# Kernel tuning notes

Measured on AMD Instinct MI355X. Metric: run time of the kernel, lower is better.

The kernel has to match this reference:

```python
import jax, jax.numpy as jnp
import numpy as np

Q, N, D, L = 4096, 50000, 5, 2


def setup_inputs() -> dict:
    key = jax.random.key(0)
    k1, k2, k3 = jax.random.split(key, 3)
    rss = jax.random.normal(k1, (Q, D), dtype=jnp.float32)
    Radio = jax.random.normal(k2, (N, D), dtype=jnp.float32)
    Loc = jax.random.normal(k3, (N, L), dtype=jnp.float32)
    sigma = jnp.ones((1,), dtype=jnp.float32)
    return {"rss": rss, "Radio": Radio, "Loc": Loc, "sigma": sigma}


def reference(rss, Radio, Loc, sigma):
    # x: [Q, 5] queries; Radio: [N, 5] reference fingerprints; Loc: [N, 2]
    x = rss.reshape(-1, D)
    # squared pairwise distances via the expanded form (no [Q,N,D] intermediate)
    x2 = jnp.sum(x * x, axis=-1, keepdims=True)            # [Q, 1]
    r2 = jnp.sum(Radio * Radio, axis=-1)                   # [N]
    d2 = x2 - 2.0 * (x @ Radio.T) + r2                     # [Q, N]
    d2 = jnp.maximum(d2, 0.0)
    sim = jnp.exp(-d2 / (2.0 * sigma[0] * sigma[0]))       # RBF kernel [Q, N]
    w = sim / jnp.sum(sim, axis=-1, keepdims=True)         # row-normalize
    l_hat = jnp.einsum('qn,nl->ql', w, Loc)                # Nadaraya-Watson [Q, 2]
    return l_hat
```

## Files before the change

### kernel.cpp

```cpp
#include <hip/hip_runtime.h>
#include <hip/hip_bf16.h>
#include <math.h>

#define QTOT   4096
#define NTOT   50000
#define NTILES 3125
#define NS     64
#define NB     16
#define QG     64
#define MAINBLOCKS (QG * NB)

#define BOFF   0u
#define BSIZE  (3125u * 512u)
#define AOFF   (BOFF + BSIZE)
#define ASIZE  (4096u * 32u)
#define ZOFF   (AOFF + ASIZE)
#define PARTOFF (ZOFF + 256u)

typedef unsigned short ushort_t;
typedef short  s16x8 __attribute__((ext_vector_type(8)));
typedef float  f32x4 __attribute__((ext_vector_type(4)));
typedef float  f2    __attribute__((ext_vector_type(2)));

#if __has_builtin(__builtin_amdgcn_exp2f)
#define EXP2F(x) __builtin_amdgcn_exp2f(x)
#else
#define EXP2F(x) exp2f(x)
#endif

static __device__ __forceinline__ f2 fma2(f2 a, f2 b, f2 c) {
#if __has_builtin(__builtin_elementwise_fma)
    return __builtin_elementwise_fma(a, b, c);
#else
    f2 r; r.x = fmaf(a.x, b.x, c.x); r.y = fmaf(a.y, b.y, c.y); return r;
#endif
}

static __device__ __forceinline__ void bsplit(float f, ushort_t& h, ushort_t& l) {
    __hip_bfloat16 hb = __float2bfloat16(f);
    float hf = __bfloat162float(hb);
    __hip_bfloat16 lb = __float2bfloat16(f - hf);
    h = *reinterpret_cast<ushort_t*>(&hb);
    l = *reinterpret_cast<ushort_t*>(&lb);
}

__global__ __launch_bounds__(256) void sknn_prep(
    const float* __restrict__ rss, const float* __restrict__ Radio,
    const float* __restrict__ sigma, char* __restrict__ ws)
{
    const int p = blockIdx.x * 256 + threadIdx.x;
    const float sg = sigma[0];
    const float g  = 1.4426950408889634f / (2.0f * sg * sg);
    const float g2 = 2.0f * g;

    if (p < NTOT) {
        float b[8]; float rr = 0.f;
        #pragma unroll
        for (int d = 0; d < 5; ++d) { float r = Radio[p*5+d]; b[d] = g2*r; rr += r*r; }
        b[5] = 1.0f; b[6] = -g * rr; b[7] = 0.0f;
        union { ushort_t u[8]; f32x4 v; } hi, lo;
        #pragma unroll
        for (int k = 0; k < 8; ++k) bsplit(b[k], hi.u[k], lo.u[k]);
        const int nt = p >> 4, nsub = p & 15;
        *(f32x4*)(ws + BOFF + (unsigned)nt*512u + (unsigned)nsub*16u)        = hi.v;
        *(f32x4*)(ws + BOFF + (unsigned)nt*512u + 256u + (unsigned)nsub*16u) = lo.v;
    }
    if (p < QTOT) {
        float a[8]; float xx = 0.f;
        #pragma unroll
        for (int d = 0; d < 5; ++d) { float x = rss[p*5+d]; a[d] = x; xx += x*x; }
        a[5] = -g * xx; a[6] = 1.0f; a[7] = 0.0f;
        union { ushort_t u[8]; f32x4 v; } hi, lo;
        #pragma unroll
        for (int k = 0; k < 8; ++k) bsplit(a[k], hi.u[k], lo.u[k]);
        *(f32x4*)(ws + AOFF + (unsigned)p*32u)       = hi.v;
        *(f32x4*)(ws + AOFF + (unsigned)p*32u + 16u) = lo.v;
    }
    if (p < 16) *(f32x4*)(ws + ZOFF + (unsigned)p*16u) = (f32x4){0.f,0.f,0.f,0.f};
}

__global__ __launch_bounds__(256, 4) void sknn_main(
    const char* __restrict__ tbl, const float* __restrict__ Loc,
    float* __restrict__ part)
{
    const int tid  = threadIdx.x;
    const int lane = tid & 63;
    const int w    = tid >> 6;
    const int qg   = blockIdx.x & (QG - 1);
    const int nb   = blockIdx.x >> 6;
    const int ns   = nb * 4 + w;
    const int qbase = qg * 64;
    const int j  = lane & 15;
    const int qd = lane >> 4;

    const unsigned abase = (qd == 3) ? (ZOFF + (unsigned)j*16u)
        : (AOFF + (unsigned)(qbase + j)*32u + (qd == 2 ? 16u : 0u));
    const unsigned astep = (qd == 3) ? 0u : 512u;
    const s16x8 a0 = *(const s16x8*)(tbl + abase);
    const s16x8 a1 = *(const s16x8*)(tbl + abase + astep);
    const s16x8 a2 = *(const s16x8*)(tbl + abase + 2u*astep);
    const s16x8 a3 = *(const s16x8*)(tbl + abase + 3u*astep);

    unsigned bofs = (qd == 3) ? (ZOFF + (unsigned)j*16u)
        : (BOFF + (unsigned)ns*512u + (qd == 1 ? 256u : 0u) + (unsigned)j*16u);
    const unsigned bstep = (qd == 3) ? 0u : (512u * NS);

    unsigned lofs = (unsigned)(ns*16 + j) * 8u;
    const char* locb = (const char*)Loc;

    f2 sm2[8]; f2 o[16];
    #pragma unroll
    for (int k = 0; k < 8;  ++k) sm2[k] = (f2){0.f, 0.f};
    #pragma unroll
    for (int k = 0; k < 16; ++k) o[k]   = (f2){0.f, 0.f};
    const f32x4 zz = {0.f, 0.f, 0.f, 0.f};

    s16x8 bcur = *(const s16x8*)(tbl + bofs);
    f2    lcur = *(const f2*)(locb + lofs);

    for (int nt = ns; nt < NTILES; nt += NS) {
        const bool has = (nt + NS) < NTILES;
        const unsigned bn = bofs + (has ? bstep : 0u);
        const unsigned ln = lofs + (has ? (unsigned)(NS*16*8) : 0u);
        const s16x8 bnx = *(const s16x8*)(tbl + bn);
        const f2    lnx = *(const f2*)(locb + ln);

        f32x4 t[4];
        t[0] = __builtin_amdgcn_mfma_f32_16x16x32_bf16(a0, bcur, zz, 0, 0, 0);
        t[1] = __builtin_amdgcn_mfma_f32_16x16x32_bf16(a1, bcur, zz, 0, 0, 0);
        t[2] = __builtin_amdgcn_mfma_f32_16x16x32_bf16(a2, bcur, zz, 0, 0, 0);
        t[3] = __builtin_amdgcn_mfma_f32_16x16x32_bf16(a3, bcur, zz, 0, 0, 0);

        #pragma unroll
        for (int qt = 0; qt < 4; ++qt) {
            const float s0 = EXP2F(t[qt][0]);
            const float s1 = EXP2F(t[qt][1]);
            const float s2 = EXP2F(t[qt][2]);
            const float s3 = EXP2F(t[qt][3]);
            sm2[qt*2+0] += (f2){s0, s1};
            sm2[qt*2+1] += (f2){s2, s3};
            o[qt*4+0] = fma2((f2){s0, s0}, lcur, o[qt*4+0]);
            o[qt*4+1] = fma2((f2){s1, s1}, lcur, o[qt*4+1]);
            o[qt*4+2] = fma2((f2){s2, s2}, lcur, o[qt*4+2]);
            o[qt*4+3] = fma2((f2){s3, s3}, lcur, o[qt*4+3]);
        }
        bcur = bnx; lcur = lnx; bofs = bn; lofs = ln;
    }

    #pragma unroll
    for (int m = 1; m <= 8; m <<= 1) {
        #pragma unroll
        for (int k = 0; k < 8; ++k) {
            sm2[k].x += __shfl_xor(sm2[k].x, m, 64);
            sm2[k].y += __shfl_xor(sm2[k].y, m, 64);
        }
        #pragma unroll
        for (int k = 0; k < 16; ++k) {
            o[k].x += __shfl_xor(o[k].x, m, 64);
            o[k].y += __shfl_xor(o[k].y, m, 64);
        }
    }

    __shared__ float red[4][3][64];
    #pragma unroll
    for (int qt = 0; qt < 4; ++qt) {
        #pragma unroll
        for (int i = 0; i < 4; ++i) {
            if (j == qt*4 + i) {
                const int ql = qt*16 + qd*4 + i;
                red[w][0][ql] = (i & 1) ? sm2[qt*2 + (i>>1)].y
                                        : sm2[qt*2 + (i>>1)].x;
                red[w][1][ql] = o[qt*4+i].x;
                red[w][2][ql] = o[qt*4+i].y;
            }
        }
    }
    __syncthreads();

    if (tid < 192) {
        const int comp = tid >> 6, ql = tid & 63;
        const float v = red[0][comp][ql] + red[1][comp][ql]
                      + red[2][comp][ql] + red[3][comp][ql];
        part[((nb * 3 + comp) << 12) + qbase + ql] = v;
    }
}

__global__ __launch_bounds__(256) void sknn_fin(
    const float* __restrict__ part, float* __restrict__ out)
{
    const int q = blockIdx.x * 256 + threadIdx.x;
    float s = 0.f, w0 = 0.f, w1 = 0.f;
    #pragma unroll
    for (int nb = 0; nb < NB; ++nb) {
        s  += part[((nb * 3 + 0) << 12) + q];
        w0 += part[((nb * 3 + 1) << 12) + q];
        w1 += part[((nb * 3 + 2) << 12) + q];
    }
    const float inv = 1.0f / s;
    out[q * 2 + 0] = w0 * inv;
    out[q * 2 + 1] = w1 * inv;
}

extern "C" void kernel_launch(void* const* d_in, const int* in_sizes, int n_in,
                              void* d_out, int out_size, void* d_ws, size_t ws_size,
                              hipStream_t stream) {
    const float* rss   = (const float*)d_in[0];
    const float* Radio = (const float*)d_in[1];
    const float* Loc   = (const float*)d_in[2];
    const float* sigma = (const float*)d_in[3];
    float* out  = (float*)d_out;
    char*  ws   = (char*)d_ws;
    float* part = (float*)(ws + PARTOFF);

    sknn_prep<<<(NTOT + 255) / 256, dim3(256), 0, stream>>>(rss, Radio, sigma, ws);
    sknn_main<<<MAINBLOCKS, dim3(256), 0, stream>>>(ws, Loc, part);
    sknn_fin<<<QTOT / 256, dim3(256), 0, stream>>>(part, out);
}
```

Before: 104.9 us.

## Move weighted Loc accumulation and row sums onto a second bf16 MFMA

```diff
diff --git a/kernel.cpp b/kernel.cpp
--- a/kernel.cpp
+++ b/kernel.cpp
@@ -9,18 +9,23 @@
 #define NB     16
 #define QG     64
 #define MAINBLOCKS (QG * NB)
+#define ASTEP_IT  (512u * NS)
+#define LTSTEP_IT (160u * NS)
+#define PREPN  (NTILES * 20)
 
 #define BOFF   0u
 #define BSIZE  (3125u * 512u)
 #define AOFF   (BOFF + BSIZE)
 #define ASIZE  (4096u * 32u)
 #define ZOFF   (AOFF + ASIZE)
-#define PARTOFF (ZOFF + 256u)
+#define LTOFF  (ZOFF + 256u)
+#define LTSIZE (3125u * 160u)
+#define PARTOFF (LTOFF + LTSIZE)
 
 typedef unsigned short ushort_t;
 typedef short  s16x8 __attribute__((ext_vector_type(8)));
+typedef short  s16x4 __attribute__((ext_vector_type(4)));
 typedef float  f32x4 __attribute__((ext_vector_type(4)));
-typedef float  f2    __attribute__((ext_vector_type(2)));
 
 #if __has_builtin(__builtin_amdgcn_exp2f)
 #define EXP2F(x) __builtin_amdgcn_exp2f(x)
@@ -28,13 +33,11 @@
 #define EXP2F(x) exp2f(x)
 #endif
 
-static __device__ __forceinline__ f2 fma2(f2 a, f2 b, f2 c) {
-#if __has_builtin(__builtin_elementwise_fma)
-    return __builtin_elementwise_fma(a, b, c);
+#if __has_builtin(__builtin_amdgcn_mfma_f32_16x16x16_bf16)
+#define MFMA16(a,b,c) __builtin_amdgcn_mfma_f32_16x16x16_bf16(a,b,c,0,0,0)
 #else
-    f2 r; r.x = fmaf(a.x, b.x, c.x); r.y = fmaf(a.y, b.y, c.y); return r;
+#define MFMA16(a,b,c) __builtin_amdgcn_mfma_f32_16x16x16bf16_1k(a,b,c,0,0,0)
 #endif
-}
 
 static __device__ __forceinline__ void bsplit(float f, ushort_t& h, ushort_t& l) {
     __hip_bfloat16 hb = __float2bfloat16(f);
@@ -44,9 +47,15 @@
     l = *reinterpret_cast<ushort_t*>(&lb);
 }
 
+static __device__ __forceinline__ ushort_t b16(float f) {
+    __hip_bfloat16 hb = __float2bfloat16(f);
+    return *reinterpret_cast<ushort_t*>(&hb);
+}
+
 __global__ __launch_bounds__(256) void sknn_prep(
     const float* __restrict__ rss, const float* __restrict__ Radio,
-    const float* __restrict__ sigma, char* __restrict__ ws)
+    const float* __restrict__ Loc, const float* __restrict__ sigma,
+    char* __restrict__ ws)
 {
     const int p = blockIdx.x * 256 + threadIdx.x;
     const float sg = sigma[0];
@@ -76,103 +85,117 @@
         *(f32x4*)(ws + AOFF + (unsigned)p*32u)       = hi.v;
         *(f32x4*)(ws + AOFF + (unsigned)p*32u + 16u) = lo.v;
     }
+    if (p < PREPN) {
+        const int T = p / 20;
+        const int c = p - T * 20;
+        const int m = c >> 2, qq = c & 3;
+        union { ushort_t u[4]; s16x4 v; } e;
+        #pragma unroll
+        for (int i = 0; i < 4; ++i) {
+            const int n = T*16 + qq*4 + i;
+            ushort_t h, l, val;
+            if (m == 0)      { bsplit(Loc[n*2+0], h, l); val = h; }
+            else if (m == 1) { bsplit(Loc[n*2+0], h, l); val = l; }
+            else if (m == 2) { bsplit(Loc[n*2+1], h, l); val = h; }
+            else if (m == 3) { bsplit(Loc[n*2+1], h, l); val = l; }
+            else             { val = b16(1.0f); }
+            e.u[i] = val;
+        }
+        *(s16x4*)(ws + LTOFF + (unsigned)T*160u + (unsigned)c*8u) = e.v;
+    }
     if (p < 16) *(f32x4*)(ws + ZOFF + (unsigned)p*16u) = (f32x4){0.f,0.f,0.f,0.f};
 }
 
+static __device__ __forceinline__ f32x4 step2(
+    const f32x4 t, const s16x4 lt, f32x4 c)
+{
+    const float s0 = EXP2F(t[0]);
+    const float s1 = EXP2F(t[1]);
+    const float s2 = EXP2F(t[2]);
+    const float s3 = EXP2F(t[3]);
+    union { ushort_t u[4]; s16x4 v; } bs;
+    bs.u[0] = b16(s0); bs.u[1] = b16(s1); bs.u[2] = b16(s2); bs.u[3] = b16(s3);
+    return MFMA16(lt, bs.v, c);
+}
+
 __global__ __launch_bounds__(256, 4) void sknn_main(
-    const char* __restrict__ tbl, const float* __restrict__ Loc,
-    float* __restrict__ part)
+    const char* __restrict__ tbl, float* __restrict__ part)
 {
     const int tid  = threadIdx.x;
     const int lane = tid & 63;
     const int w    = tid >> 6;
-    const int qg   = blockIdx.x & (QG - 1);
-    const int nb   = blockIdx.x >> 6;
+    const int nb   = blockIdx.x & (NB - 1);
+    const int qg   = blockIdx.x >> 4;
     const int ns   = nb * 4 + w;
     const int qbase = qg * 64;
     const int j  = lane & 15;
     const int qd = lane >> 4;
 
-    const unsigned abase = (qd == 3) ? (ZOFF + (unsigned)j*16u)
-        : (AOFF + (unsigned)(qbase + j)*32u + (qd == 2 ? 16u : 0u));
-    const unsigned astep = (qd == 3) ? 0u : 512u;
-    const s16x8 a0 = *(const s16x8*)(tbl + abase);
-    const s16x8 a1 = *(const s16x8*)(tbl + abase + astep);
-    const s16x8 a2 = *(const s16x8*)(tbl + abase + 2u*astep);
-    const s16x8 a3 = *(const s16x8*)(tbl + abase + 3u*astep);
-
-    unsigned bofs = (qd == 3) ? (ZOFF + (unsigned)j*16u)
-        : (BOFF + (unsigned)ns*512u + (qd == 1 ? 256u : 0u) + (unsigned)j*16u);
-    const unsigned bstep = (qd == 3) ? 0u : (512u * NS);
-
-    unsigned lofs = (unsigned)(ns*16 + j) * 8u;
-    const char* locb = (const char*)Loc;
-
-    f2 sm2[8]; f2 o[16];
+    const unsigned qb = (qd == 3) ? (ZOFF + (unsigned)j*16u)
+        : (AOFF + (unsigned)(qbase + j)*32u + (qd == 1 ? 16u : 0u));
+    const unsigned qs = (qd == 3) ? 0u : 512u;
+    const s16x8 bq0 = *(const s16x8*)(tbl + qb);
+    const s16x8 bq1 = *(const s16x8*)(tbl + qb + qs);
+    const s16x8 bq2 = *(const s16x8*)(tbl + qb + 2u*qs);
+    const s16x8 bq3 = *(const s16x8*)(tbl + qb + 3u*qs);
+
+    unsigned aofs = (qd == 3) ? (ZOFF + (unsigned)j*16u)
+        : (BOFF + (unsigned)ns*512u + (qd == 2 ? 256u : 0u) + (unsigned)j*16u);
+    const unsigned astep = (qd == 3) ? 0u : ASTEP_IT;
+
+    unsigned ltofs = (j < 5) ? (LTOFF + (unsigned)ns*160u + (unsigned)(j*4+qd)*8u)
+                             : ZOFF;
+    const unsigned ltstep = (j < 5) ? LTSTEP_IT : 0u;
+
+    f32x4 c2[4];
     #pragma unroll
-    for (int k = 0; k < 8;  ++k) sm2[k] = (f2){0.f, 0.f};
-    #pragma unroll
-    for (int k = 0; k < 16; ++k) o[k]   = (f2){0.f, 0.f};
+    for (int k = 0; k < 4; ++k) c2[k] = (f32x4){0.f, 0.f, 0.f, 0.f};
     const f32x4 zz = {0.f, 0.f, 0.f, 0.f};
 
-    s16x8 bcur = *(const s16x8*)(tbl + bofs);
-    f2    lcur = *(const f2*)(locb + lofs);
-
-    for (int nt = ns; nt < NTILES; nt += NS) {
-        const bool has = (nt + NS) < NTILES;
-        const unsigned bn = bofs + (has ? bstep : 0u);
-        const unsigned ln = lofs + (has ? (unsigned)(NS*16*8) : 0u);
-        const s16x8 bnx = *(const s16x8*)(tbl + bn);
-        const f2    lnx = *(const f2*)(locb + ln);
-
-        f32x4 t[4];
-        t[0] = __builtin_amdgcn_mfma_f32_16x16x32_bf16(a0, bcur, zz, 0, 0, 0);
-        t[1] = __builtin_amdgcn_mfma_f32_16x16x32_bf16(a1, bcur, zz, 0, 0, 0);
-        t[2] = __builtin_amdgcn_mfma_f32_16x16x32_bf16(a2, bcur, zz, 0, 0, 0);
-        t[3] = __builtin_amdgcn_mfma_f32_16x16x32_bf16(a3, bcur, zz, 0, 0, 0);
-
+    s16x8 acur = *(const s16x8*)(tbl + aofs);
+    s16x4 lcur = *(const s16x4*)(tbl + ltofs);
+
+    int nt = ns;
+    while (nt + NS < NTILES) {
+        aofs  += astep;
+        ltofs += ltstep;
+        const s16x8 anx = *(const s16x8*)(tbl + aofs);
+        const s16x4 lnx = *(const s16x4*)(tbl + ltofs);
+
+        const f32x4 t0 = __builtin_amdgcn_mfma_f32_16x16x32_bf16(acur, bq0, zz, 0, 0, 0);
+        const f32x4 t1 = __builtin_amdgcn_mfma_f32_16x16x32_bf16(acur, bq1, zz, 0, 0, 0);
+        const f32x4 t2 = __builtin_amdgcn_mfma_f32_16x16x32_bf16(acur, bq2, zz, 0, 0, 0);
+        const f32x4 t3 = __builtin_amdgcn_mfma_f32_16x16x32_bf16(acur, bq3, zz, 0, 0, 0);
+        c2[0] = step2(t0, lcur, c2[0]);
+        c2[1] = step2(t1, lcur, c2[1]);
+        c2[2] = step2(t2, lcur, c2[2]);
+        c2[3] = step2(t3, lcur, c2[3]);
+
+        acur = anx; lcur = lnx;
+        nt += NS;
+    }
+    {
+        const f32x4 t0 = __builtin_amdgcn_mfma_f32_16x16x32_bf16(acur, bq0, zz, 0, 0, 0);
+        const f32x4 t1 = __builtin_amdgcn_mfma_f32_16x16x32_bf16(acur, bq1, zz, 0, 0, 0);
+        const f32x4 t2 = __builtin_amdgcn_mfma_f32_16x16x32_bf16(acur, bq2, zz, 0, 0, 0);
+        const f32x4 t3 = __builtin_amdgcn_mfma_f32_16x16x32_bf16(acur, bq3, zz, 0, 0, 0);
+        c2[0] = step2(t0, lcur, c2[0]);
+        c2[1] = step2(t1, lcur, c2[1]);
+        c2[2] = step2(t2, lcur, c2[2]);
+        c2[3] = step2(t3, lcur, c2[3]);
+    }
+
+    __shared__ float red[4][3][64];
+    if (qd == 0) {
         #pragma unroll
         for (int qt = 0; qt < 4; ++qt) {
-            const float s0 = EXP2F(t[qt][0]);
-            const float s1 = EXP2F(t[qt][1]);
-            const float s2 = EXP2F(t[qt][2]);
-            const float s3 = EXP2F(t[qt][3]);
-            sm2[qt*2+0] += (f2){s0, s1};
-            sm2[qt*2+1] += (f2){s2, s3};
-            o[qt*4+0] = fma2((f2){s0, s0}, lcur, o[qt*4+0]);
-            o[qt*4+1] = fma2((f2){s1, s1}, lcur, o[qt*4+1]);
-            o[qt*4+2] = fma2((f2){s2, s2}, lcur, o[qt*4+2]);
-            o[qt*4+3] = fma2((f2){s3, s3}, lcur, o[qt*4+3]);
+            red[w][1][qt*16 + j] = c2[qt][0] + c2[qt][1];
+            red[w][2][qt*16 + j] = c2[qt][2] + c2[qt][3];
         }
-        bcur = bnx; lcur = lnx; bofs = bn; lofs = ln;
-    }
-
-    #pragma unroll
-    for (int m = 1; m <= 8; m <<= 1) {
-        #pragma unroll
-        for (int k = 0; k < 8; ++k) {
-            sm2[k].x += __shfl_xor(sm2[k].x, m, 64);
-            sm2[k].y += __shfl_xor(sm2[k].y, m, 64);
-        }
-        #pragma unroll
-        for (int k = 0; k < 16; ++k) {
-            o[k].x += __shfl_xor(o[k].x, m, 64);
-            o[k].y += __shfl_xor(o[k].y, m, 64);
-        }
-    }
-
-    __shared__ float red[4][3][64];
-    #pragma unroll
-    for (int qt = 0; qt < 4; ++qt) {
-        #pragma unroll
-        for (int i = 0; i < 4; ++i) {
-            if (j == qt*4 + i) {
-                const int ql = qt*16 + qd*4 + i;
-                red[w][0][ql] = (i & 1) ? sm2[qt*2 + (i>>1)].y
-                                        : sm2[qt*2 + (i>>1)].x;
-                red[w][1][ql] = o[qt*4+i].x;
-                red[w][2][ql] = o[qt*4+i].y;
-            }
+    } else if (qd == 1) {
+        #pragma unroll
+        for (int qt = 0; qt < 4; ++qt) {
+            red[w][0][qt*16 + j] = c2[qt][0];
         }
     }
     __syncthreads();
@@ -212,7 +235,7 @@
     char*  ws   = (char*)d_ws;
     float* part = (float*)(ws + PARTOFF);
 
-    sknn_prep<<<(NTOT + 255) / 256, dim3(256), 0, stream>>>(rss, Radio, sigma, ws);
-    sknn_main<<<MAINBLOCKS, dim3(256), 0, stream>>>(ws, Loc, part);
+    sknn_prep<<<(PREPN + 255) / 256, dim3(256), 0, stream>>>(rss, Radio, Loc, sigma, ws);
+    sknn_main<<<MAINBLOCKS, dim3(256), 0, stream>>>(ws, part);
     sknn_fin<<<QTOT / 256, dim3(256), 0, stream>>>(part, out);
 }
```

Result: faster. 96.71 us (-7.8%).
